# Kernel tuning notes

Measured on AMD Instinct MI355X. Metric: run time of the kernel, lower is better.

The kernel has to match this reference:

```python
import jax, jax.numpy as jnp
import numpy as np

B, T, D, H = 8, 1024, 512, 8
CH = D // H          # chunk_size = d_model // num_heads
PAD = 0              # pad_token_id
MAX_TRANS = 1024     # translen cap from source
NINF = float('-inf')


def setup_inputs() -> dict:
    key = jax.random.key(0)
    ks = jax.random.split(key, 8)
    features = jax.random.normal(ks[0], (B, T, D), jnp.float32)
    pos_embed = jax.random.normal(ks[1], (B, T, D), jnp.float32)
    tokens = jax.random.randint(ks[2], (B, T), 0, 32000, dtype=jnp.int32)
    Wq = jax.random.normal(ks[3], (D, 2 * D), jnp.float32) * 0.02
    bq = jnp.zeros((D,), jnp.float32)
    Wk = jax.random.normal(ks[4], (D, 2 * D), jnp.float32) * 0.02
    bk = jnp.zeros((D,), jnp.float32)
    Wg = jax.random.normal(ks[5], (H, 2 * D), jnp.float32) * 0.02
    bg = jnp.zeros((H,), jnp.float32)
    return dict(features=features, pos_embed=pos_embed, tokens=tokens,
                Wq=Wq, bq=bq, Wk=Wk, bk=bk, Wg=Wg, bg=bg)


def _safe_log_softmax(x, axis):
    # matches torch F.log_softmax followed by re-masking: rows that are all -inf stay -inf
    m = jnp.max(x, axis=axis, keepdims=True)
    allinf = jnp.isneginf(m)
    m_safe = jnp.where(allinf, 0.0, m)
    lse = m_safe + jnp.log(jnp.sum(jnp.exp(x - m_safe), axis=axis, keepdims=True))
    lse = jnp.where(allinf, 0.0, lse)
    return x - lse


def _safe_logsumexp(x, axis):
    # matches the custom logsumexp helper in the source (all -inf -> -inf, no nan)
    m = jnp.max(x, axis=axis)
    mask = jnp.isneginf(m)
    m_safe = jnp.where(mask, 0.0, m)
    s = jnp.sum(jnp.exp(x - jnp.expand_dims(m_safe, axis)), axis=axis)
    return jnp.log(jnp.where(mask, 1.0, s)) + jnp.where(mask, NINF, m_safe)


def reference(features, pos_embed, tokens, Wq, bq, Wk, bk, Wg, bg):
    # features_withpos = cat(decoder_out, link positional embedding)  -> [B, T, 2D]
    f = jnp.concatenate([features, pos_embed], axis=-1)
    q = (f @ Wq.T + bq).reshape(B, T, H, CH)
    k = (f @ Wk.T + bk).reshape(B, T, H, CH)
    log_gates = jax.nn.log_softmax(f @ Wg.T + bg, axis=-1)  # [B, T, H]
    # einsum 'bicf,bjcf->bijc' with c = head chunk
    scores = jnp.einsum('bihc,bjhc->bijh', q, k) / np.float32(np.sqrt(CH))  # [B,T,T,H]

    translen = min(MAX_TRANS, T - 1)
    n_valid = jnp.sum(tokens != PAD, axis=-1)  # [B]
    # banded indices: position i links to positions i+1 .. i+translen
    band_idx = jnp.arange(T)[:, None] + jnp.arange(translen)[None, :] + 1  # [T, translen]
    invalid = band_idx[None, :, :] >= n_valid[:, None, None]               # [B, T, translen]
    idx_c = jnp.where(invalid, 0, band_idx[None, :, :])
    idx_full = jnp.broadcast_to(idx_c[..., None], (B, T, translen, H))
    extract = jnp.take_along_axis(scores, idx_full, axis=2)                # [B,T,translen,H]
    extract = jnp.where(invalid[..., None], NINF, extract)
    # normalize over transition axis, then mask fully-invalid rows back to -inf
    extract = _safe_log_softmax(extract, axis=2)
    nouse = jnp.all(invalid, axis=-1)                                      # [B, T]
    extract = jnp.where(nouse[:, :, None, None], NINF, extract)
    # head-gated logsumexp over heads -> banded links [B, T, translen]
    links_band = _safe_logsumexp(extract + log_gates[:, :, None, :], axis=-1)
    # restore_valid_links: scatter band back to full [B, T, T] (-inf elsewhere)
    rel = jnp.arange(T)[None, :] - jnp.arange(T)[:, None] - 1              # [T, T]
    valid = (rel >= 0) & (rel < translen)
    rel_c = jnp.clip(rel, 0, translen - 1)
    rel_full = jnp.broadcast_to(rel_c[None, :, :], (B, T, T))
    out = jnp.take_along_axis(links_band, rel_full, axis=2)
    return jnp.where(valid[None, :, :], out, NINF)
```

## Files before the change

### kernel.cpp

```cpp
#include <hip/hip_runtime.h>
#include <math.h>

#define BATCH 8
#define T 1024
#define NH 8
#define NROW 8192
#define NEG_INF (-INFINITY)
#define SENT (-1.0e30f)
#define SC 0.180336880f
#define LOG2E 1.442695041f

typedef __attribute__((ext_vector_type(8))) short short8;
typedef __attribute__((ext_vector_type(4))) float f32x4;

__device__ __forceinline__ ushort f2bf(float x) {
  uint u = __float_as_uint(x);
  return (ushort)((u + 0x7FFFu + ((u >> 16) & 1u)) >> 16);
}
__device__ __forceinline__ uint pack2(float a, float b) {
  return (uint)f2bf(a) | ((uint)f2bf(b) << 16);
}
__device__ __forceinline__ void gl_lds16(const ushort* g, ushort* l) {
  __builtin_amdgcn_global_load_lds(
      (const __attribute__((address_space(1))) unsigned int*)g,
      (__attribute__((address_space(3))) unsigned int*)l, 16, 0, 0);
}

__global__ __launch_bounds__(256) void k_nvalid(const int* __restrict__ tokens,
                                                int* __restrict__ nv) {
  int b = blockIdx.x, t = threadIdx.x;
  int cnt = 0;
  for (int i = t; i < T; i += 256) cnt += (tokens[b * T + i] != 0) ? 1 : 0;
  __shared__ int s[256];
  s[t] = cnt;
  __syncthreads();
  for (int st = 128; st > 0; st >>= 1) {
    if (t < st) s[t] += s[t + st];
    __syncthreads();
  }
  if (t == 0) nv[b] = s[0];
}

__global__ __launch_bounds__(256) void k_prep_w(const float* __restrict__ Wq,
                                                const float* __restrict__ Wk,
                                                ushort* __restrict__ Wbf) {
  const int gid = blockIdx.x * 256 + threadIdx.x;
  const int e0 = gid * 8;
  const int n = e0 >> 10, k = e0 & 1023;
  const float* src = (n < 512) ? (Wq + (size_t)n * 1024 + k)
                               : (Wk + (size_t)(n - 512) * 1024 + k);
  float4 a = *(const float4*)src;
  float4 b = *(const float4*)(src + 4);
  uint4 o;
  o.x = pack2(a.x, a.y); o.y = pack2(a.z, a.w);
  o.z = pack2(b.x, b.y); o.w = pack2(b.z, b.w);
  *(uint4*)(Wbf + (size_t)n * 1024 + k) = o;
}

__global__ __launch_bounds__(256) void k_prep_fg(
    const float* __restrict__ feat, const float* __restrict__ pos,
    const float* __restrict__ Wg, const float* __restrict__ bg,
    ushort* __restrict__ fbf, float* __restrict__ gout) {
  __shared__ __align__(16) float Ws[8192];
  const int tid = threadIdx.x;
#pragma unroll
  for (int u = 0; u < 8; ++u)
    ((float4*)Ws)[u * 256 + tid] = ((const float4*)Wg)[u * 256 + tid];
  __syncthreads();

  const int w = tid >> 6, l = tid & 63;
  const int c0 = l * 16;
  const int row0 = blockIdx.x * 8 + w * 2;

  float4 f[2][4];
#pragma unroll
  for (int r = 0; r < 2; ++r) {
    const int row = row0 + r;
    const float* src = (c0 < 512) ? (feat + (size_t)row * 512 + c0)
                                  : (pos + (size_t)row * 512 + (c0 - 512));
#pragma unroll
    for (int q4 = 0; q4 < 4; ++q4) f[r][q4] = *(const float4*)(src + q4 * 4);
    uint4 o0, o1;
    o0.x = pack2(f[r][0].x, f[r][0].y); o0.y = pack2(f[r][0].z, f[r][0].w);
    o0.z = pack2(f[r][1].x, f[r][1].y); o0.w = pack2(f[r][1].z, f[r][1].w);
    o1.x = pack2(f[r][2].x, f[r][2].y); o1.y = pack2(f[r][2].z, f[r][2].w);
    o1.z = pack2(f[r][3].x, f[r][3].y); o1.w = pack2(f[r][3].z, f[r][3].w);
    *(uint4*)(fbf + (size_t)row * 1024 + c0) = o0;
    *(uint4*)(fbf + (size_t)row * 1024 + c0 + 8) = o1;
  }

  float s[2][8];
#pragma unroll
  for (int h = 0; h < 8; ++h) {
    const float* wg = Ws + h * 1024 + c0;
    float4 w0 = *(const float4*)(wg + 0);
    float4 w1 = *(const float4*)(wg + 4);
    float4 w2 = *(const float4*)(wg + 8);
    float4 w3 = *(const float4*)(wg + 12);
#pragma unroll
    for (int r = 0; r < 2; ++r)
      s[r][h] = f[r][0].x * w0.x + f[r][0].y * w0.y + f[r][0].z * w0.z + f[r][0].w * w0.w
              + f[r][1].x * w1.x + f[r][1].y * w1.y + f[r][1].z * w1.z + f[r][1].w * w1.w
              + f[r][2].x * w2.x + f[r][2].y * w2.y + f[r][2].z * w2.z + f[r][2].w * w2.w
              + f[r][3].x * w3.x + f[r][3].y * w3.y + f[r][3].z * w3.z + f[r][3].w * w3.w;
  }
#pragma unroll
  for (int m = 1; m < 64; m <<= 1)
#pragma unroll
    for (int r = 0; r < 2; ++r)
#pragma unroll
      for (int h = 0; h < 8; ++h) s[r][h] += __shfl_xor(s[r][h], m, 64);
  if (l == 0) {
#pragma unroll
    for (int r = 0; r < 2; ++r) {
      float lg[8], mx = -1e30f;
#pragma unroll
      for (int h = 0; h < 8; ++h) { lg[h] = s[r][h] + bg[h]; mx = fmaxf(mx, lg[h]); }
      float sum = 0.f;
#pragma unroll
      for (int h = 0; h < 8; ++h) sum += __expf(lg[h] - mx);
      const float lse = mx + __logf(sum);
#pragma unroll
      for (int h = 0; h < 8; ++h) gout[(size_t)(row0 + r) * 8 + h] = lg[h] - lse;
    }
  }
}

__global__ __launch_bounds__(256) void k_gemm(
    const ushort* __restrict__ fbf, const ushort* __restrict__ Wbf,
    const float* __restrict__ bq, const float* __restrict__ bk,
    ushort* __restrict__ qbuf, ushort* __restrict__ kbuf) {
  const int g = blockIdx.x + 8 * blockIdx.y;
  const int wid = (g & 7) * 64 + (g >> 3);
  const int n0 = (wid & 7) * 128;
  const int m0 = (wid >> 3) * 128;
  const int tid = threadIdx.x;
  const int w = tid >> 6, l = tid & 63;
  const int lo = l & 15, quad = l >> 4;
  const int wm0 = (w >> 1) * 64, wn0 = (w & 1) * 64;

  __shared__ ushort As[128 * 64];
  __shared__ ushort Bs[128 * 64];

  f32x4 acc[4][4];
#pragma unroll
  for (int i = 0; i < 4; ++i)
#pragma unroll
    for (int j = 0; j < 4; ++j) acc[i][j] = (f32x4){0.f, 0.f, 0.f, 0.f};

  const int c8 = (tid & 7) * 8;
  const int r0 = tid >> 3;
  ushort* lA = As + (size_t)w * 512;
  ushort* lB = Bs + (size_t)w * 512;

  for (int k0 = 0; k0 < 1024; k0 += 64) {
    __syncthreads();
#pragma unroll
    for (int u = 0; u < 4; ++u) {
      gl_lds16(fbf + (size_t)(m0 + u * 32 + r0) * 1024 + k0 + c8, lA + u * 2048);
      gl_lds16(Wbf + (size_t)(n0 + u * 32 + r0) * 1024 + k0 + c8, lB + u * 2048);
    }
    __syncthreads();
#pragma unroll
    for (int kk = 0; kk < 2; ++kk) {
      short8 af[4], bfr[4];
#pragma unroll
      for (int mi = 0; mi < 4; ++mi)
        af[mi] = *(const short8*)(As + (size_t)(wm0 + mi * 16 + lo) * 64 + kk * 32 + quad * 8);
#pragma unroll
      for (int ni = 0; ni < 4; ++ni)
        bfr[ni] = *(const short8*)(Bs + (size_t)(wn0 + ni * 16 + lo) * 64 + kk * 32 + quad * 8);
#pragma unroll
      for (int mi = 0; mi < 4; ++mi)
#pragma unroll
        for (int ni = 0; ni < 4; ++ni)
          acc[mi][ni] = __builtin_amdgcn_mfma_f32_16x16x32_bf16(bfr[ni], af[mi], acc[mi][ni], 0, 0, 0);
    }
  }

  float4 bias4[4];
#pragma unroll
  for (int ni = 0; ni < 4; ++ni) {
    const int gn = n0 + wn0 + ni * 16 + quad * 4;
    bias4[ni] = *(const float4*)((gn < 512) ? (bq + gn) : (bk + gn - 512));
  }
#pragma unroll
  for (int mi = 0; mi < 4; ++mi) {
    const int m = m0 + wm0 + mi * 16 + lo;
#pragma unroll
    for (int ni = 0; ni < 4; ++ni) {
      const int gn = n0 + wn0 + ni * 16 + quad * 4;
      ushort* dst = (gn < 512) ? (qbuf + (size_t)m * 512 + gn)
                               : (kbuf + (size_t)m * 512 + gn - 512);
      ushort4 o;
      o.x = f2bf(acc[mi][ni][0] + bias4[ni].x);
      o.y = f2bf(acc[mi][ni][1] + bias4[ni].y);
      o.z = f2bf(acc[mi][ni][2] + bias4[ni].z);
      o.w = f2bf(acc[mi][ni][3] + bias4[ni].w);
      *(ushort4*)dst = o;
    }
  }
}

__global__ __launch_bounds__(256) void k_pass1(
    const ushort* __restrict__ q, const ushort* __restrict__ kv,
    const float* __restrict__ g, const int* __restrict__ nvp,
    float* __restrict__ Wt) {
  const int it = blockIdx.x, h = blockIdx.y, b = blockIdx.z;
  const int nv = nvp[b];
  const int i0 = it * 64;
  const int tid = threadIdx.x;
  const int w = tid >> 6, l = tid & 63;
  const int lo = l & 15, quad = l >> 4;

  __shared__ ushort Ks[2][64 * 64];

  const int i = i0 + w * 16 + lo;
  const ushort* qp = q + (size_t)(b * T + i) * 512 + h * 64 + quad * 8;
  const short8 a0 = *(const short8*)qp;
  const short8 a1 = *(const short8*)(qp + 32);

  float lsum = 0.f;
  const int ntile = ((nv + 63) >> 6) - it;

  if (ntile > 0) {
    auto stage = [&](int buf, int jt) {
#pragma unroll
      for (int u = 0; u < 2; ++u) {
        const int s = u * 256 + tid;
        const int row = s >> 3, c = s & 7;
        gl_lds16(kv + (size_t)(b * T + jt * 64 + row) * 512 + h * 64 + ((c ^ (row & 7)) * 8),
                 Ks[buf] + (size_t)(u * 256 + w * 64) * 8);
      }
    };
    stage(0, it);
    __syncthreads();
    for (int s = 0; s < ntile; ++s) {
      if (s + 1 < ntile) stage((s + 1) & 1, it + s + 1);
      const ushort* kbase = Ks[s & 1];
      const int j0 = (it + s) * 64;
      const bool diag = (s == 0);
      const bool masked = diag | (j0 + 64 > nv);
#pragma unroll
      for (int ni = 0; ni < 4; ++ni) {
        if (diag && ni < w) continue;
        const int rw = ni * 16 + lo;
        const short8 b0 = *(const short8*)(kbase + (size_t)rw * 64 + ((quad ^ (rw & 7)) * 8));
        const short8 b1 = *(const short8*)(kbase + (size_t)rw * 64 + (((4 + quad) ^ (rw & 7)) * 8));
        f32x4 acc = (f32x4){0.f, 0.f, 0.f, 0.f};
        acc = __builtin_amdgcn_mfma_f32_16x16x32_bf16(b0, a0, acc, 0, 0, 0);
        acc = __builtin_amdgcn_mfma_f32_16x16x32_bf16(b1, a1, acc, 0, 0, 0);
        if (!masked) {
#pragma unroll
          for (int r = 0; r < 4; ++r) lsum += __builtin_amdgcn_exp2f(acc[r] * SC);
        } else {
          const int jb = j0 + ni * 16 + quad * 4;
#pragma unroll
          for (int r = 0; r < 4; ++r) {
            const int j = jb + r;
            if (j > i && j < nv) lsum += __builtin_amdgcn_exp2f(acc[r] * SC);
          }
        }
      }
      __syncthreads();
    }
  }

  lsum += __shfl_xor(lsum, 16, 64);
  lsum += __shfl_xor(lsum, 32, 64);
  if (quad == 0) {
    const size_t row = (size_t)(b * T) + i;
    Wt[(size_t)h * NROW + row] =
        (lsum > 0.f) ? (g[row * 8 + h] - __logf(lsum)) : NEG_INF;
  }
}

__global__ __launch_bounds__(256) void k_pass2(
    const ushort* __restrict__ q, const ushort* __restrict__ kv,
    const float* __restrict__ Wt, const int* __restrict__ nvp,
    float* __restrict__ out) {
  const int jt = blockIdx.x, it = blockIdx.y, b = blockIdx.z;
  const int nv = nvp[b];
  const int i0 = it * 64, j0 = jt * 64;
  const int tid = threadIdx.x;

  if (jt < it || j0 >= nv) {
    const int r0 = tid >> 4, c0 = (tid & 15) * 4;
    float4 v; v.x = v.y = v.z = v.w = SENT;
#pragma unroll
    for (int u = 0; u < 4; ++u)
      *(float4*)(out + ((size_t)(b * T + i0 + r0 + u * 16)) * T + j0 + c0) = v;
    return;
  }

  const int w = tid >> 6, l = tid & 63;
  const int lo = l & 15, quad = l >> 4;
  const int i = i0 + w * 16 + lo;

  __shared__ ushort Ks[64 * 512];

#pragma unroll
  for (int u = 0; u < 16; ++u) {
    const int row = u * 4 + w;
    gl_lds16(kv + (size_t)(b * T + j0 + row) * 512 + ((l ^ (row & 7)) * 8),
             Ks + (size_t)(u * 256 + w * 64) * 8);
  }

  const ushort* qb = q + (size_t)(b * T + i) * 512 + quad * 8;
  short8 qa0[8], qa1[8];
  float wl[8];
#pragma unroll
  for (int h = 0; h < 8; ++h) {
    qa0[h] = *(const short8*)(qb + h * 64);
    qa1[h] = *(const short8*)(qb + h * 64 + 32);
    wl[h] = Wt[(size_t)h * NROW + b * T + i] * LOG2E;
  }

  float se[4][4];
#pragma unroll
  for (int a = 0; a < 4; ++a)
#pragma unroll
    for (int c = 0; c < 4; ++c) se[a][c] = 0.f;

  __syncthreads();

#pragma unroll
  for (int h = 0; h < 8; ++h) {
#pragma unroll
    for (int ni = 0; ni < 4; ++ni) {
      const int rw = ni * 16 + lo;
      const int cs0 = (h * 8 + quad) ^ (rw & 7);
      const int cs1 = (h * 8 + 4 + quad) ^ (rw & 7);
      const short8 b0 = *(const short8*)(Ks + (size_t)rw * 512 + cs0 * 8);
      const short8 b1 = *(const short8*)(Ks + (size_t)rw * 512 + cs1 * 8);
      f32x4 acc = (f32x4){0.f, 0.f, 0.f, 0.f};
      acc = __builtin_amdgcn_mfma_f32_16x16x32_bf16(b0, qa0[h], acc, 0, 0, 0);
      acc = __builtin_amdgcn_mfma_f32_16x16x32_bf16(b1, qa1[h], acc, 0, 0, 0);
#pragma unroll
      for (int r = 0; r < 4; ++r)
        se[ni][r] += __builtin_amdgcn_exp2f(acc[r] * SC + wl[h]);
    }
  }

  const size_t orow = ((size_t)(b * T + i)) * T;
#pragma unroll
  for (int ni = 0; ni < 4; ++ni) {
    const int jb = j0 + ni * 16 + quad * 4;
    float4 v;
    v.x = (jb + 0 > i && jb + 0 < nv) ? fmaxf(__logf(se[ni][0]), SENT) : SENT;
    v.y = (jb + 1 > i && jb + 1 < nv) ? fmaxf(__logf(se[ni][1]), SENT) : SENT;
    v.z = (jb + 2 > i && jb + 2 < nv) ? fmaxf(__logf(se[ni][2]), SENT) : SENT;
    v.w = (jb + 3 > i && jb + 3 < nv) ? fmaxf(__logf(se[ni][3]), SENT) : SENT;
    *(float4*)(out + orow + jb) = v;
  }
}

extern "C" void kernel_launch(void* const* d_in, const int* in_sizes, int n_in,
                              void* d_out, int out_size, void* d_ws, size_t ws_size,
                              hipStream_t stream) {
  (void)in_sizes; (void)n_in; (void)out_size; (void)ws_size;
  const float* feat = (const float*)d_in[0];
  const float* pos  = (const float*)d_in[1];
  const int* tokens = (const int*)d_in[2];
  const float* Wq = (const float*)d_in[3];
  const float* bq = (const float*)d_in[4];
  const float* Wk = (const float*)d_in[5];
  const float* bk = (const float*)d_in[6];
  const float* Wg = (const float*)d_in[7];
  const float* bg = (const float*)d_in[8];
  float* out = (float*)d_out;

  ushort* qbuf = (ushort*)d_ws;
  ushort* kbuf = qbuf + (size_t)NROW * 512;
  ushort* Wbf  = kbuf + (size_t)NROW * 512;
  float*  gbuf = (float*)(Wbf + (size_t)1024 * 1024);
  float*  Wt   = gbuf + (size_t)NROW * NH;
  int*    nv   = (int*)(Wt + (size_t)NH * NROW);

  ushort* fbf = (ushort*)d_out;

  k_nvalid<<<dim3(BATCH), dim3(256), 0, stream>>>(tokens, nv);
  k_prep_w<<<dim3(512), dim3(256), 0, stream>>>(Wq, Wk, Wbf);
  k_prep_fg<<<dim3(1024), dim3(256), 0, stream>>>(feat, pos, Wg, bg, fbf, gbuf);
  k_gemm<<<dim3(8, 64), dim3(256), 0, stream>>>(fbf, Wbf, bq, bk, qbuf, kbuf);
  k_pass1<<<dim3(16, NH, BATCH), dim3(256), 0, stream>>>(qbuf, kbuf, gbuf, nv, Wt);
  k_pass2<<<dim3(16, 16, BATCH), dim3(256), 0, stream>>>(qbuf, kbuf, Wt, nv, out);
}
```

Before: 189.8 us.

## Merge prep kernels, double-buffer GEMM staging, use 32x32 MFMA in pass2

```diff
diff --git a/kernel.cpp b/kernel.cpp
--- a/kernel.cpp
+++ b/kernel.cpp
@@ -12,6 +12,7 @@
 
 typedef __attribute__((ext_vector_type(8))) short short8;
 typedef __attribute__((ext_vector_type(4))) float f32x4;
+typedef __attribute__((ext_vector_type(16))) float f32x16;
 
 __device__ __forceinline__ ushort f2bf(float x) {
   uint u = __float_as_uint(x);
@@ -26,103 +27,103 @@
       (__attribute__((address_space(3))) unsigned int*)l, 16, 0, 0);
 }
 
-__global__ __launch_bounds__(256) void k_nvalid(const int* __restrict__ tokens,
-                                                int* __restrict__ nv) {
-  int b = blockIdx.x, t = threadIdx.x;
-  int cnt = 0;
-  for (int i = t; i < T; i += 256) cnt += (tokens[b * T + i] != 0) ? 1 : 0;
-  __shared__ int s[256];
-  s[t] = cnt;
-  __syncthreads();
-  for (int st = 128; st > 0; st >>= 1) {
-    if (t < st) s[t] += s[t + st];
+__global__ __launch_bounds__(256) void k_prep(
+    const float* __restrict__ feat, const float* __restrict__ pos,
+    const int* __restrict__ tokens,
+    const float* __restrict__ Wq, const float* __restrict__ Wk,
+    const float* __restrict__ Wg, const float* __restrict__ bg,
+    ushort* __restrict__ fbf, ushort* __restrict__ Wbf,
+    float* __restrict__ gout, int* __restrict__ nvout) {
+  const int bid = blockIdx.x;
+  const int tid = threadIdx.x;
+
+  if (bid < 1024) {
+    __shared__ __align__(16) float Ws[8192];
+#pragma unroll
+    for (int u = 0; u < 8; ++u)
+      ((float4*)Ws)[u * 256 + tid] = ((const float4*)Wg)[u * 256 + tid];
     __syncthreads();
-  }
-  if (t == 0) nv[b] = s[0];
-}
-
-__global__ __launch_bounds__(256) void k_prep_w(const float* __restrict__ Wq,
-                                                const float* __restrict__ Wk,
-                                                ushort* __restrict__ Wbf) {
-  const int gid = blockIdx.x * 256 + threadIdx.x;
-  const int e0 = gid * 8;
-  const int n = e0 >> 10, k = e0 & 1023;
-  const float* src = (n < 512) ? (Wq + (size_t)n * 1024 + k)
-                               : (Wk + (size_t)(n - 512) * 1024 + k);
-  float4 a = *(const float4*)src;
-  float4 b = *(const float4*)(src + 4);
-  uint4 o;
-  o.x = pack2(a.x, a.y); o.y = pack2(a.z, a.w);
-  o.z = pack2(b.x, b.y); o.w = pack2(b.z, b.w);
-  *(uint4*)(Wbf + (size_t)n * 1024 + k) = o;
-}
-
-__global__ __launch_bounds__(256) void k_prep_fg(
-    const float* __restrict__ feat, const float* __restrict__ pos,
-    const float* __restrict__ Wg, const float* __restrict__ bg,
-    ushort* __restrict__ fbf, float* __restrict__ gout) {
-  __shared__ __align__(16) float Ws[8192];
-  const int tid = threadIdx.x;
-#pragma unroll
-  for (int u = 0; u < 8; ++u)
-    ((float4*)Ws)[u * 256 + tid] = ((const float4*)Wg)[u * 256 + tid];
-  __syncthreads();
-
-  const int w = tid >> 6, l = tid & 63;
-  const int c0 = l * 16;
-  const int row0 = blockIdx.x * 8 + w * 2;
-
-  float4 f[2][4];
-#pragma unroll
-  for (int r = 0; r < 2; ++r) {
-    const int row = row0 + r;
-    const float* src = (c0 < 512) ? (feat + (size_t)row * 512 + c0)
-                                  : (pos + (size_t)row * 512 + (c0 - 512));
-#pragma unroll
-    for (int q4 = 0; q4 < 4; ++q4) f[r][q4] = *(const float4*)(src + q4 * 4);
-    uint4 o0, o1;
-    o0.x = pack2(f[r][0].x, f[r][0].y); o0.y = pack2(f[r][0].z, f[r][0].w);
-    o0.z = pack2(f[r][1].x, f[r][1].y); o0.w = pack2(f[r][1].z, f[r][1].w);
-    o1.x = pack2(f[r][2].x, f[r][2].y); o1.y = pack2(f[r][2].z, f[r][2].w);
-    o1.z = pack2(f[r][3].x, f[r][3].y); o1.w = pack2(f[r][3].z, f[r][3].w);
-    *(uint4*)(fbf + (size_t)row * 1024 + c0) = o0;
-    *(uint4*)(fbf + (size_t)row * 1024 + c0 + 8) = o1;
-  }
-
-  float s[2][8];
-#pragma unroll
-  for (int h = 0; h < 8; ++h) {
-    const float* wg = Ws + h * 1024 + c0;
-    float4 w0 = *(const float4*)(wg + 0);
-    float4 w1 = *(const float4*)(wg + 4);
-    float4 w2 = *(const float4*)(wg + 8);
-    float4 w3 = *(const float4*)(wg + 12);
-#pragma unroll
-    for (int r = 0; r < 2; ++r)
-      s[r][h] = f[r][0].x * w0.x + f[r][0].y * w0.y + f[r][0].z * w0.z + f[r][0].w * w0.w
-              + f[r][1].x * w1.x + f[r][1].y * w1.y + f[r][1].z * w1.z + f[r][1].w * w1.w
-              + f[r][2].x * w2.x + f[r][2].y * w2.y + f[r][2].z * w2.z + f[r][2].w * w2.w
-              + f[r][3].x * w3.x + f[r][3].y * w3.y + f[r][3].z * w3.z + f[r][3].w * w3.w;
-  }
-#pragma unroll
-  for (int m = 1; m < 64; m <<= 1)
-#pragma unroll
-    for (int r = 0; r < 2; ++r)
-#pragma unroll
-      for (int h = 0; h < 8; ++h) s[r][h] += __shfl_xor(s[r][h], m, 64);
-  if (l == 0) {
+
+    const int w = tid >> 6, l = tid & 63;
+    const int c0 = l * 16;
+    const int row0 = bid * 8 + w * 2;
+
+    float4 f[2][4];
 #pragma unroll
     for (int r = 0; r < 2; ++r) {
-      float lg[8], mx = -1e30f;
-#pragma unroll
-      for (int h = 0; h < 8; ++h) { lg[h] = s[r][h] + bg[h]; mx = fmaxf(mx, lg[h]); }
-      float sum = 0.f;
-#pragma unroll
-      for (int h = 0; h < 8; ++h) sum += __expf(lg[h] - mx);
-      const float lse = mx + __logf(sum);
-#pragma unroll
-      for (int h = 0; h < 8; ++h) gout[(size_t)(row0 + r) * 8 + h] = lg[h] - lse;
-    }
+      const int row = row0 + r;
+      const float* src = (c0 < 512) ? (feat + (size_t)row * 512 + c0)
+                                    : (pos + (size_t)row * 512 + (c0 - 512));
+#pragma unroll
+      for (int q4 = 0; q4 < 4; ++q4) f[r][q4] = *(const float4*)(src + q4 * 4);
+      uint4 o0, o1;
+      o0.x = pack2(f[r][0].x, f[r][0].y); o0.y = pack2(f[r][0].z, f[r][0].w);
+      o0.z = pack2(f[r][1].x, f[r][1].y); o0.w = pack2(f[r][1].z, f[r][1].w);
+      o1.x = pack2(f[r][2].x, f[r][2].y); o1.y = pack2(f[r][2].z, f[r][2].w);
+      o1.z = pack2(f[r][3].x, f[r][3].y); o1.w = pack2(f[r][3].z, f[r][3].w);
+      *(uint4*)(fbf + (size_t)row * 1024 + c0) = o0;
+      *(uint4*)(fbf + (size_t)row * 1024 + c0 + 8) = o1;
+    }
+
+    float s[2][8];
+#pragma unroll
+    for (int h = 0; h < 8; ++h) {
+      const float* wg = Ws + h * 1024 + c0;
+      float4 w0 = *(const float4*)(wg + 0);
+      float4 w1 = *(const float4*)(wg + 4);
+      float4 w2 = *(const float4*)(wg + 8);
+      float4 w3 = *(const float4*)(wg + 12);
+#pragma unroll
+      for (int r = 0; r < 2; ++r)
+        s[r][h] = f[r][0].x * w0.x + f[r][0].y * w0.y + f[r][0].z * w0.z + f[r][0].w * w0.w
+                + f[r][1].x * w1.x + f[r][1].y * w1.y + f[r][1].z * w1.z + f[r][1].w * w1.w
+                + f[r][2].x * w2.x + f[r][2].y * w2.y + f[r][2].z * w2.z + f[r][2].w * w2.w
+                + f[r][3].x * w3.x + f[r][3].y * w3.y + f[r][3].z * w3.z + f[r][3].w * w3.w;
+    }
+#pragma unroll
+    for (int m = 1; m < 64; m <<= 1)
+#pragma unroll
+      for (int r = 0; r < 2; ++r)
+#pragma unroll
+        for (int h = 0; h < 8; ++h) s[r][h] += __shfl_xor(s[r][h], m, 64);
+    if (l == 0) {
+#pragma unroll
+      for (int r = 0; r < 2; ++r) {
+        float lg[8], mx = -1e30f;
+#pragma unroll
+        for (int h = 0; h < 8; ++h) { lg[h] = s[r][h] + bg[h]; mx = fmaxf(mx, lg[h]); }
+        float sum = 0.f;
+#pragma unroll
+        for (int h = 0; h < 8; ++h) sum += __expf(lg[h] - mx);
+        const float lse = mx + __logf(sum);
+#pragma unroll
+        for (int h = 0; h < 8; ++h) gout[(size_t)(row0 + r) * 8 + h] = lg[h] - lse;
+      }
+    }
+  } else if (bid < 1536) {
+    const int gid = (bid - 1024) * 256 + tid;
+    const int e0 = gid * 8;
+    const int n = e0 >> 10, k = e0 & 1023;
+    const float* src = (n < 512) ? (Wq + (size_t)n * 1024 + k)
+                                 : (Wk + (size_t)(n - 512) * 1024 + k);
+    float4 a = *(const float4*)src;
+    float4 b = *(const float4*)(src + 4);
+    uint4 o;
+    o.x = pack2(a.x, a.y); o.y = pack2(a.z, a.w);
+    o.z = pack2(b.x, b.y); o.w = pack2(b.z, b.w);
+    *(uint4*)(Wbf + (size_t)n * 1024 + k) = o;
+  } else {
+    const int b = bid - 1536;
+    int cnt = 0;
+    for (int i = tid; i < T; i += 256) cnt += (tokens[b * T + i] != 0) ? 1 : 0;
+    __shared__ int s[256];
+    s[tid] = cnt;
+    __syncthreads();
+    for (int st = 128; st > 0; st >>= 1) {
+      if (tid < st) s[tid] += s[tid + st];
+      __syncthreads();
+    }
+    if (tid == 0) nvout[b] = s[0];
   }
 }
 
@@ -139,8 +140,8 @@
   const int lo = l & 15, quad = l >> 4;
   const int wm0 = (w >> 1) * 64, wn0 = (w & 1) * 64;
 
-  __shared__ ushort As[128 * 64];
-  __shared__ ushort Bs[128 * 64];
+  __shared__ ushort As[2][128 * 64];
+  __shared__ ushort Bs[2][128 * 64];
 
   f32x4 acc[4][4];
 #pragma unroll
@@ -150,32 +151,40 @@
 
   const int c8 = (tid & 7) * 8;
   const int r0 = tid >> 3;
-  ushort* lA = As + (size_t)w * 512;
-  ushort* lB = Bs + (size_t)w * 512;
-
+
+  auto stage = [&](int buf, int k0) {
+#pragma unroll
+    for (int u = 0; u < 4; ++u) {
+      gl_lds16(fbf + (size_t)(m0 + u * 32 + r0) * 1024 + k0 + c8,
+               As[buf] + (size_t)w * 512 + u * 2048);
+      gl_lds16(Wbf + (size_t)(n0 + u * 32 + r0) * 1024 + k0 + c8,
+               Bs[buf] + (size_t)w * 512 + u * 2048);
+    }
+  };
+
+  stage(0, 0);
+  int cur = 0;
   for (int k0 = 0; k0 < 1024; k0 += 64) {
     __syncthreads();
-#pragma unroll
-    for (int u = 0; u < 4; ++u) {
-      gl_lds16(fbf + (size_t)(m0 + u * 32 + r0) * 1024 + k0 + c8, lA + u * 2048);
-      gl_lds16(Wbf + (size_t)(n0 + u * 32 + r0) * 1024 + k0 + c8, lB + u * 2048);
-    }
-    __syncthreads();
+    if (k0 + 64 < 1024) stage(cur ^ 1, k0 + 64);
+    const ushort* pA = As[cur];
+    const ushort* pB = Bs[cur];
 #pragma unroll
     for (int kk = 0; kk < 2; ++kk) {
       short8 af[4], bfr[4];
 #pragma unroll
       for (int mi = 0; mi < 4; ++mi)
-        af[mi] = *(const short8*)(As + (size_t)(wm0 + mi * 16 + lo) * 64 + kk * 32 + quad * 8);
+        af[mi] = *(const short8*)(pA + (size_t)(wm0 + mi * 16 + lo) * 64 + kk * 32 + quad * 8);
 #pragma unroll
       for (int ni = 0; ni < 4; ++ni)
-        bfr[ni] = *(const short8*)(Bs + (size_t)(wn0 + ni * 16 + lo) * 64 + kk * 32 + quad * 8);
+        bfr[ni] = *(const short8*)(pB + (size_t)(wn0 + ni * 16 + lo) * 64 + kk * 32 + quad * 8);
 #pragma unroll
       for (int mi = 0; mi < 4; ++mi)
 #pragma unroll
         for (int ni = 0; ni < 4; ++ni)
           acc[mi][ni] = __builtin_amdgcn_mfma_f32_16x16x32_bf16(bfr[ni], af[mi], acc[mi][ni], 0, 0, 0);
     }
+    cur ^= 1;
   }
 
   float4 bias4[4];
@@ -294,64 +303,85 @@
   }
 
   const int w = tid >> 6, l = tid & 63;
-  const int lo = l & 15, quad = l >> 4;
-  const int i = i0 + w * 16 + lo;
+  const int lc = l & 31, hi = l >> 5;
+  const int ih = (w & 1) * 32, jh = (w >> 1) * 32;
+  const int i = i0 + ih + lc;
 
   __shared__ ushort Ks[64 * 512];
 
 #pragma unroll
   for (int u = 0; u < 16; ++u) {
     const int row = u * 4 + w;
-    gl_lds16(kv + (size_t)(b * T + j0 + row) * 512 + ((l ^ (row & 7)) * 8),
-             Ks + (size_t)(u * 256 + w * 64) * 8);
-  }
-
-  const ushort* qb = q + (size_t)(b * T + i) * 512 + quad * 8;
-  short8 qa0[8], qa1[8];
+    gl_lds16(kv + (size_t)(b * T + j0 + row) * 512 + ((l ^ (row & 15)) * 8),
+             Ks + (size_t)row * 512);
+  }
+
+  const ushort* qb = q + (size_t)(b * T + i) * 512;
+  short8 qf[8][4];
   float wl[8];
 #pragma unroll
   for (int h = 0; h < 8; ++h) {
-    qa0[h] = *(const short8*)(qb + h * 64);
-    qa1[h] = *(const short8*)(qb + h * 64 + 32);
+#pragma unroll
+    for (int kh = 0; kh < 4; ++kh)
+      qf[h][kh] = *(const short8*)(qb + h * 64 + kh * 16 + hi * 8);
     wl[h] = Wt[(size_t)h * NROW + b * T + i] * LOG2E;
   }
 
-  float se[4][4];
-#pragma unroll
-  for (int a = 0; a < 4; ++a)
-#pragma unroll
-    for (int c = 0; c < 4; ++c) se[a][c] = 0.f;
+  float se[16];
+#pragma unroll
+  for (int r = 0; r < 16; ++r) se[r] = 0.f;
 
   __syncthreads();
 
+  if (jt == it && jh + 32 <= ih) {
+    const size_t orow = ((size_t)(b * T + i)) * T;
+    float4 v; v.x = v.y = v.z = v.w = SENT;
+#pragma unroll
+    for (int g2 = 0; g2 < 4; ++g2)
+      *(float4*)(out + orow + j0 + jh + g2 * 8 + hi * 4) = v;
+    return;
+  }
+
+  const ushort* krow = Ks + (size_t)(jh + lc) * 512;
+  const int sw = lc & 15;
 #pragma unroll
   for (int h = 0; h < 8; ++h) {
-#pragma unroll
-    for (int ni = 0; ni < 4; ++ni) {
-      const int rw = ni * 16 + lo;
-      const int cs0 = (h * 8 + quad) ^ (rw & 7);
-      const int cs1 = (h * 8 + 4 + quad) ^ (rw & 7);
-      const short8 b0 = *(const short8*)(Ks + (size_t)rw * 512 + cs0 * 8);
-      const short8 b1 = *(const short8*)(Ks + (size_t)rw * 512 + cs1 * 8);
-      f32x4 acc = (f32x4){0.f, 0.f, 0.f, 0.f};
-      acc = __builtin_amdgcn_mfma_f32_16x16x32_bf16(b0, qa0[h], acc, 0, 0, 0);
-      acc = __builtin_amdgcn_mfma_f32_16x16x32_bf16(b1, qa1[h], acc, 0, 0, 0);
-#pragma unroll
-      for (int r = 0; r < 4; ++r)
-        se[ni][r] += __builtin_amdgcn_exp2f(acc[r] * SC + wl[h]);
-    }
+    f32x16 acc;
+#pragma unroll
+    for (int r = 0; r < 16; ++r) acc[r] = 0.f;
+#pragma unroll
+    for (int kh = 0; kh < 4; ++kh) {
+      const short8 af = *(const short8*)(krow + ((size_t)((h * 8 + kh * 2 + hi) ^ sw) * 8));
+      acc = __builtin_amdgcn_mfma_f32_32x32x16_bf16(af, qf[h][kh], acc, 0, 0, 0);
+    }
+#pragma unroll
+    for (int r = 0; r < 16; ++r)
+      se[r] += __builtin_amdgcn_exp2f(acc[r] * SC + wl[h]);
   }
 
   const size_t orow = ((size_t)(b * T + i)) * T;
-#pragma unroll
-  for (int ni = 0; ni < 4; ++ni) {
-    const int jb = j0 + ni * 16 + quad * 4;
-    float4 v;
-    v.x = (jb + 0 > i && jb + 0 < nv) ? fmaxf(__logf(se[ni][0]), SENT) : SENT;
-    v.y = (jb + 1 > i && jb + 1 < nv) ? fmaxf(__logf(se[ni][1]), SENT) : SENT;
-    v.z = (jb + 2 > i && jb + 2 < nv) ? fmaxf(__logf(se[ni][2]), SENT) : SENT;
-    v.w = (jb + 3 > i && jb + 3 < nv) ? fmaxf(__logf(se[ni][3]), SENT) : SENT;
-    *(float4*)(out + orow + jb) = v;
+  const bool maskfree = (j0 + jh > i0 + ih + 31) && (j0 + jh + 32 <= nv);
+  if (maskfree) {
+#pragma unroll
+    for (int g2 = 0; g2 < 4; ++g2) {
+      float4 v;
+      v.x = fmaxf(__logf(se[g2 * 4 + 0]), SENT);
+      v.y = fmaxf(__logf(se[g2 * 4 + 1]), SENT);
+      v.z = fmaxf(__logf(se[g2 * 4 + 2]), SENT);
+      v.w = fmaxf(__logf(se[g2 * 4 + 3]), SENT);
+      *(float4*)(out + orow + j0 + jh + g2 * 8 + hi * 4) = v;
+    }
+  } else {
+#pragma unroll
+    for (int g2 = 0; g2 < 4; ++g2) {
+      const int jb = j0 + jh + g2 * 8 + hi * 4;
+      float4 v;
+      v.x = (jb + 0 > i && jb + 0 < nv) ? fmaxf(__logf(se[g2 * 4 + 0]), SENT) : SENT;
+      v.y = (jb + 1 > i && jb + 1 < nv) ? fmaxf(__logf(se[g2 * 4 + 1]), SENT) : SENT;
+      v.z = (jb + 2 > i && jb + 2 < nv) ? fmaxf(__logf(se[g2 * 4 + 2]), SENT) : SENT;
+      v.w = (jb + 3 > i && jb + 3 < nv) ? fmaxf(__logf(se[g2 * 4 + 3]), SENT) : SENT;
+      *(float4*)(out + orow + jb) = v;
+    }
   }
 }
 
@@ -379,9 +409,8 @@
 
   ushort* fbf = (ushort*)d_out;
 
-  k_nvalid<<<dim3(BATCH), dim3(256), 0, stream>>>(tokens, nv);
-  k_prep_w<<<dim3(512), dim3(256), 0, stream>>>(Wq, Wk, Wbf);
-  k_prep_fg<<<dim3(1024), dim3(256), 0, stream>>>(feat, pos, Wg, bg, fbf, gbuf);
+  k_prep<<<dim3(1544), dim3(256), 0, stream>>>(feat, pos, tokens, Wq, Wk, Wg, bg,
+                                               fbf, Wbf, gbuf, nv);
   k_gemm<<<dim3(8, 64), dim3(256), 0, stream>>>(fbf, Wbf, bq, bk, qbuf, kbuf);
   k_pass1<<<dim3(16, NH, BATCH), dim3(256), 0, stream>>>(qbuf, kbuf, gbuf, nv, Wt);
   k_pass2<<<dim3(16, 16, BATCH), dim3(256), 0, stream>>>(qbuf, kbuf, Wt, nv, out);
```

Result: slower. 194.4 us (+2.4%).
